# Optimization experiments

Hardware: AMD Instinct MI355X
Metric: run time of the kernel (lower is better)

The kernel has to match this reference:

```python
import jax, jax.numpy as jnp
import numpy as np

MASK_ID = 8192


def setup_inputs() -> dict:
    key = jax.random.key(0)
    k1, k2, k3, k4 = jax.random.split(key, 4)
    B, S, D = 8, 512, 1024
    x = jax.random.normal(k1, (B, S, D), dtype=jnp.float32) * 0.05
    embedding = jax.random.normal(k2, (B, S, D), dtype=jnp.float32) * 0.05
    tok = jax.random.randint(k3, (B, S), 0, MASK_ID)
    is_masked = jax.random.uniform(k4, (B, S)) < 0.15
    masked_target = jnp.where(is_masked, MASK_ID, tok).astype(jnp.int64)
    return {"x": x, "embedding": embedding, "masked_target": masked_target}


def reference(x, embedding, masked_target):
    # x, embedding: [B, S, D]; masked_target: [B, S]
    B, S, D = x.shape
    mask = (masked_target == MASK_ID)                      # [B, S]
    # numerator logit: f . m per position
    numer = jnp.sum(embedding * x, axis=-1)                # [B, S]
    # denominator: each query f against ALL B*S hidden states
    keys = x.reshape(B * S, D)                             # [N, D]
    scores = jnp.einsum('bsd,nd->bsn', embedding, keys)    # [B, S, N]
    lse = jax.nn.logsumexp(scores, axis=-1)                # [B, S]
    # log(exp(numer) / sum(exp(scores))) == numer - lse
    per_tok = numer - lse
    count = jnp.sum(mask).astype(x.dtype)
    loss = jnp.sum(jnp.where(mask, per_tok, jnp.zeros_like(per_tok)))
    return -(loss / count)
```

## Files before the change

kernel.cpp:

```cpp
#include <hip/hip_runtime.h>
#include <hip/hip_bf16.h>
#include <stdint.h>

constexpr int N_TOK  = 4096;
constexpr int D_DIM  = 1024;
constexpr int MASK_ID_V = 8192;

constexpr int BM2  = 256;
constexpr int KIT  = D_DIM / 128;
constexpr int NSL2 = N_TOK / BM2;
constexpr int NPART = NSL2 * 4;

constexpr float SCALE   = 64.0f;
constexpr float INVSC2  = 1.0f / (SCALE * SCALE);

constexpr int BM = 128, BN = 128, BK = 64;
constexpr int KST = D_DIM / BK;
constexpr int NSLICE_FB = 8;
constexpr int SLICE_W   = N_TOK / NSLICE_FB;
constexpr int CTS       = SLICE_W / BN;
constexpr int LDW       = BK + 8;
constexpr int NPART_FB  = NSLICE_FB * 2;

constexpr int FIN_BLOCKS = 256;

typedef __attribute__((ext_vector_type(4)))  float f32x4;
typedef __attribute__((ext_vector_type(16))) float f32x16;
typedef __attribute__((ext_vector_type(8)))  short bf16x8;
typedef __attribute__((ext_vector_type(8)))  int   i32x8;

__device__ __forceinline__ uint32_t pk2bf(float lo, float hi) {
    union { float f; uint32_t u; } a, b;
    a.f = lo; b.f = hi;
    uint32_t ua = (a.u + 0x7fffu + ((a.u >> 16) & 1u)) >> 16;
    uint32_t ub = (b.u + 0x7fffu + ((b.u >> 16) & 1u)) >> 16;
    return ua | (ub << 16);
}

__device__ __forceinline__ void async16(void* lds, const void* g) {
    __builtin_amdgcn_global_load_lds(
        (const __attribute__((address_space(1))) uint32_t*)g,
        (__attribute__((address_space(3))) uint32_t*)lds,
        16, 0, 0);
}

#define BAR do { __builtin_amdgcn_s_barrier(); __builtin_amdgcn_sched_barrier(0); } while (0)

__device__ __forceinline__ uint pk4fp8(float4 v) {
    int w = __builtin_amdgcn_cvt_pk_fp8_f32(v.x * SCALE, v.y * SCALE, 0, false);
    w = __builtin_amdgcn_cvt_pk_fp8_f32(v.z * SCALE, v.w * SCALE, w, true);
    return (uint)w;
}

__global__ __launch_bounds__(256) void conv_fp8(
    const float* __restrict__ x, const float* __restrict__ e,
    unsigned char* __restrict__ xb8, unsigned char* __restrict__ eb8)
{
    constexpr int NC = N_TOK * D_DIM / 16;
    const int t0 = blockIdx.x * blockDim.x + threadIdx.x;
    const int stride = gridDim.x * blockDim.x;
    for (int c = t0; c < NC; c += stride) {
        const float4* px = (const float4*)x + (size_t)c * 4;
        uint4 o;
        o.x = pk4fp8(px[0]); o.y = pk4fp8(px[1]);
        o.z = pk4fp8(px[2]); o.w = pk4fp8(px[3]);
        ((uint4*)xb8)[c] = o;

        const float4* pe = (const float4*)e + (size_t)c * 4;
        uint4 q;
        q.x = pk4fp8(pe[0]); q.y = pk4fp8(pe[1]);
        q.z = pk4fp8(pe[2]); q.w = pk4fp8(pe[3]);
        ((uint4*)eb8)[c] = q;
    }
}

__device__ __forceinline__ i32x8 ld_frag(const unsigned char* base, int o0, int o1) {
    uint4 u = *(const uint4*)(base + o0);
    uint4 v = *(const uint4*)(base + o1);
    i32x8 r = { (int)u.x, (int)u.y, (int)u.z, (int)u.w,
                (int)v.x, (int)v.y, (int)v.z, (int)v.w };
    return r;
}

#define MFMA8(A_, B_, C_) __builtin_amdgcn_mfma_scale_f32_32x32x64_f8f6f4( \
    A_, B_, C_, 0, 0, 0, 127, 0, 127)

__global__ __launch_bounds__(1024, 4) void nce_gemm_fp8(
    const unsigned char* __restrict__ xb8,
    const unsigned char* __restrict__ eb8,
    float* __restrict__ numer,
    float* __restrict__ ps)
{
    __shared__ unsigned char As[2][32768];
    __shared__ unsigned char Bs[2][32768];

    const int bid   = blockIdx.x;
    const int sw    = (bid & 7) * 32 + (bid >> 3);
    const int chunk = sw >> 4, win = sw & 15;
    const int rb    = (chunk & 3) * 4 + (win & 3);
    const int cs    = (chunk >> 2) * 4 + (win >> 2);
    const int row0  = rb * BM2;
    const int col0  = cs * BM2;

    const int tid  = threadIdx.x;
    const int lane = tid & 63;
    const int wid  = tid >> 6;
    const int wr   = wid >> 2;
    const int wc   = wid & 3;
    const int l31  = lane & 31;
    const int lg   = lane >> 5;

    const int q0_ = wid * 128 + lane;
    const int q1_ = q0_ + 64;
    const int r0_ = q0_ >> 3, c0_ = (q0_ & 7) ^ (r0_ & 7);
    const int r1_ = q1_ >> 3, c1_ = (q1_ & 7) ^ (r1_ & 7);
    const unsigned char* gA0 = eb8 + (size_t)(row0 + r0_) * D_DIM + c0_ * 16;
    const unsigned char* gA1 = eb8 + (size_t)(row0 + r1_) * D_DIM + c1_ * 16;
    const unsigned char* gB0 = xb8 + (size_t)(col0 + r0_) * D_DIM + c0_ * 16;
    const unsigned char* gB1 = xb8 + (size_t)(col0 + r1_) * D_DIM + c1_ * 16;

    const int rA = wr * 64 + l31;
    const int pA = (lg * 2) ^ (rA & 7);
    const int rB = wc * 64 + l31;
    const int pB = (lg * 2) ^ (rB & 7);
    int offA[2][2], offB[2][2];
#pragma unroll
    for (int ks = 0; ks < 2; ++ks)
#pragma unroll
        for (int j = 0; j < 2; ++j) {
            offA[ks][j] = rA * 128 + ((pA ^ (ks << 2) ^ j) << 4);
            offB[ks][j] = rB * 128 + ((pB ^ (ks << 2) ^ j) << 4);
        }

    f32x16 acc00, acc01, acc10, acc11;
#pragma unroll
    for (int i = 0; i < 16; ++i) { acc00[i] = 0.f; acc01[i] = 0.f; acc10[i] = 0.f; acc11[i] = 0.f; }

    async16(As[0] + wid * 2048,        gA0);
    async16(As[0] + wid * 2048 + 1024, gA1);
    async16(Bs[0] + wid * 2048,        gB0);
    async16(Bs[0] + wid * 2048 + 1024, gB1);

#pragma unroll 1
    for (int kt = 0; kt < KIT; ++kt) {
        const int c = kt & 1, n = c ^ 1;

        asm volatile("s_waitcnt vmcnt(0)" ::: "memory");
        BAR;

        if (kt < KIT - 1) {
            const int ko = (kt + 1) * 128;
            async16(As[n] + wid * 2048,        gA0 + ko);
            async16(As[n] + wid * 2048 + 1024, gA1 + ko);
            async16(Bs[n] + wid * 2048,        gB0 + ko);
            async16(Bs[n] + wid * 2048 + 1024, gB1 + ko);
        }

        const unsigned char* Ab = As[c];
        const unsigned char* Bb = Bs[c];
#pragma unroll
        for (int ks = 0; ks < 2; ++ks) {
            i32x8 a0 = ld_frag(Ab,        offA[ks][0], offA[ks][1]);
            i32x8 a1 = ld_frag(Ab + 4096, offA[ks][0], offA[ks][1]);
            i32x8 b0 = ld_frag(Bb,        offB[ks][0], offB[ks][1]);
            i32x8 b1 = ld_frag(Bb + 4096, offB[ks][0], offB[ks][1]);
            __builtin_amdgcn_s_setprio(1);
            acc00 = MFMA8(a0, b0, acc00);
            acc01 = MFMA8(a0, b1, acc01);
            acc10 = MFMA8(a1, b0, acc10);
            acc11 = MFMA8(a1, b1, acc11);
            __builtin_amdgcn_s_setprio(0);
        }
    }

    const int c0g = col0 + wc * 64 + l31;
    const int c1g = c0g + 32;

#pragma unroll
    for (int reg = 0; reg < 16; ++reg) {
        const int rif = (reg & 3) + 8 * (reg >> 2) + 4 * lg;
#pragma unroll
        for (int fr = 0; fr < 2; ++fr) {
            const int row_g = row0 + wr * 64 + fr * 32 + rif;
            const float v0 = (fr ? acc10[reg] : acc00[reg]) * INVSC2;
            const float v1 = (fr ? acc11[reg] : acc01[reg]) * INVSC2;
            if (row_g == c0g) numer[row_g] = v0;
            if (row_g == c1g) numer[row_g] = v1;
            float s = __expf(v0) + __expf(v1);
#pragma unroll
            for (int off = 1; off <= 16; off <<= 1)
                s += __shfl_xor(s, off, 64);
            if (l31 == 0)
                ps[row_g * NPART + cs * 4 + wc] = s;
        }
    }
}

__global__ __launch_bounds__(256) void nce_finish_a2(
    const int* __restrict__ tgt,
    const float* __restrict__ numer,
    const float* __restrict__ ps,
    float* __restrict__ bl_loss,
    float* __restrict__ bl_cnt)
{
    const int tid  = threadIdx.x;
    const int lane = tid & 63;
    const int wv   = tid >> 6;
    const int waves_total = gridDim.x * 4;

    float loss = 0.f, cnt = 0.f;

    for (int row = blockIdx.x * 4 + wv; row < N_TOK; row += waves_total) {
        if (tgt[row] != MASK_ID_V) continue;
        float sv = (lane < NPART) ? ps[row * NPART + lane] : 0.f;
#pragma unroll
        for (int off = 32; off; off >>= 1) sv += __shfl_xor(sv, off, 64);
        if (lane == 0) {
            loss += numer[row] - __logf(sv);
            cnt  += 1.f;
        }
    }

    __shared__ float sl[4], sc[4];
    if (lane == 0) { sl[wv] = loss; sc[wv] = cnt; }
    __syncthreads();
    if (tid == 0) {
        bl_loss[blockIdx.x] = sl[0] + sl[1] + sl[2] + sl[3];
        bl_cnt[blockIdx.x]  = sc[0] + sc[1] + sc[2] + sc[3];
    }
}

__global__ __launch_bounds__(256) void nce_finish_a(
    const int* __restrict__ tgt,
    const float* __restrict__ numer,
    const float* __restrict__ pm,
    const float* __restrict__ ps,
    float* __restrict__ bl_loss,
    float* __restrict__ bl_cnt,
    int npart)
{
    const int tid  = threadIdx.x;
    const int lane = tid & 63;
    const int wv   = tid >> 6;
    const int waves_total = gridDim.x * 4;

    float loss = 0.f, cnt = 0.f;

    for (int row = blockIdx.x * 4 + wv; row < N_TOK; row += waves_total) {
        if (tgt[row] != MASK_ID_V) continue;
        float pmv = -3.0e38f, psv = 0.f;
        if (lane < npart) {
            pmv = pm[row * npart + lane];
            psv = ps[row * npart + lane];
        }
        float m = pmv;
#pragma unroll
        for (int off = 32; off; off >>= 1) m = fmaxf(m, __shfl_xor(m, off, 64));
        float sv = psv * __expf(pmv - m);
#pragma unroll
        for (int off = 32; off; off >>= 1) sv += __shfl_xor(sv, off, 64);
        if (lane == 0) {
            loss += numer[row] - (m + __logf(sv));
            cnt  += 1.f;
        }
    }

    __shared__ float sl[4], sc[4];
    if (lane == 0) { sl[wv] = loss; sc[wv] = cnt; }
    __syncthreads();
    if (tid == 0) {
        bl_loss[blockIdx.x] = sl[0] + sl[1] + sl[2] + sl[3];
        bl_cnt[blockIdx.x]  = sc[0] + sc[1] + sc[2] + sc[3];
    }
}

__global__ __launch_bounds__(256) void nce_finish_b(
    const float* __restrict__ bl_loss,
    const float* __restrict__ bl_cnt,
    float* __restrict__ out, int nblk)
{
    const int tid = threadIdx.x;
    float l = 0.f, c = 0.f;
    for (int i = tid; i < nblk; i += 256) { l += bl_loss[i]; c += bl_cnt[i]; }
    __shared__ float sl[256], sc[256];
    sl[tid] = l; sc[tid] = c;
    __syncthreads();
    for (int off = 128; off; off >>= 1) {
        if (tid < off) { sl[tid] += sl[tid + off]; sc[tid] += sc[tid + off]; }
        __syncthreads();
    }
    if (tid == 0) out[0] = -(sl[0] / sc[0]);
}

__global__ __launch_bounds__(256, 2) void nce_gemm_fb(
    const float* __restrict__ x, const float* __restrict__ emb,
    float* __restrict__ numer, float* __restrict__ pm, float* __restrict__ ps)
{
    __shared__ ushort At[BM][LDW];
    __shared__ ushort Bt[BN][LDW];

    const int rb = blockIdx.x, cs = blockIdx.y;
    const int row0 = rb * BM, col0 = cs * SLICE_W;
    const int tid = threadIdx.x, lane = tid & 63, wid = tid >> 6;
    const int wr = wid >> 1, wc = wid & 1, l15 = lane & 15, lhi = lane >> 4;

    float m_run[16], s_run[16];
#pragma unroll
    for (int i = 0; i < 16; ++i) { m_run[i] = -3.0e38f; s_run[i] = 0.0f; }

    for (int ct = 0; ct < CTS; ++ct) {
        const int colt0 = col0 + ct * BN;
        f32x4 acc[4][4];
#pragma unroll
        for (int a = 0; a < 4; ++a)
#pragma unroll
            for (int b = 0; b < 4; ++b) acc[a][b] = f32x4{0.f,0.f,0.f,0.f};

#pragma unroll 1
        for (int kt = 0; kt < KST; ++kt) {
            __syncthreads();
#pragma unroll
            for (int i = 0; i < 4; ++i) {
                const int chunk = tid + i * 256;
                const int r = chunk >> 3, c8 = (chunk & 7) << 3;
                const float* ga = emb + (size_t)(row0 + r) * D_DIM + kt * BK + c8;
                float4 a0 = *(const float4*)(ga); float4 a1 = *(const float4*)(ga + 4);
                uint4 pa;
                pa.x = pk2bf(a0.x, a0.y); pa.y = pk2bf(a0.z, a0.w);
                pa.z = pk2bf(a1.x, a1.y); pa.w = pk2bf(a1.z, a1.w);
                *(uint4*)&At[r][c8] = pa;
                const float* gb = x + (size_t)(colt0 + r) * D_DIM + kt * BK + c8;
                float4 b0 = *(const float4*)(gb); float4 b1 = *(const float4*)(gb + 4);
                uint4 pb;
                pb.x = pk2bf(b0.x, b0.y); pb.y = pk2bf(b0.z, b0.w);
                pb.z = pk2bf(b1.x, b1.y); pb.w = pk2bf(b1.z, b1.w);
                *(uint4*)&Bt[r][c8] = pb;
            }
            __syncthreads();
#pragma unroll
            for (int kp = 0; kp < 2; ++kp) {
                const int ko = kp * 32 + lhi * 8;
                bf16x8 af[4], bfr[4];
#pragma unroll
                for (int mi = 0; mi < 4; ++mi)
                    af[mi] = *(const bf16x8*)&At[wr*64 + mi*16 + l15][ko];
#pragma unroll
                for (int ni = 0; ni < 4; ++ni)
                    bfr[ni] = *(const bf16x8*)&Bt[wc*64 + ni*16 + l15][ko];
#pragma unroll
                for (int mi = 0; mi < 4; ++mi)
#pragma unroll
                    for (int ni = 0; ni < 4; ++ni)
                        acc[mi][ni] = __builtin_amdgcn_mfma_f32_16x16x32_bf16(
                            af[mi], bfr[ni], acc[mi][ni], 0, 0, 0);
            }
        }

#pragma unroll
        for (int mi = 0; mi < 4; ++mi)
#pragma unroll
            for (int r = 0; r < 4; ++r) {
                const int row_g = row0 + wr*64 + mi*16 + lhi*4 + r;
#pragma unroll
                for (int ni = 0; ni < 4; ++ni) {
                    const int col_g = colt0 + wc*64 + ni*16 + l15;
                    if (row_g == col_g) numer[row_g] = acc[mi][ni][r];
                }
                const int idx = mi * 4 + r;
                const float v0 = acc[mi][0][r], v1 = acc[mi][1][r];
                const float v2 = acc[mi][2][r], v3 = acc[mi][3][r];
                const float mx = fmaxf(fmaxf(v0, v1), fmaxf(v2, v3));
                const float mn = fmaxf(m_run[idx], mx);
                const float scale = __expf(m_run[idx] - mn);
                s_run[idx] = s_run[idx] * scale
                           + __expf(v0 - mn) + __expf(v1 - mn)
                           + __expf(v2 - mn) + __expf(v3 - mn);
                m_run[idx] = mn;
            }
    }

#pragma unroll
    for (int idx = 0; idx < 16; ++idx) {
        float m = m_run[idx], s = s_run[idx];
#pragma unroll
        for (int off = 1; off < 16; off <<= 1) {
            const float mo = __shfl_xor(m, off, 64);
            const float so = __shfl_xor(s, off, 64);
            const float mn = fmaxf(m, mo);
            s = s * __expf(m - mn) + so * __expf(mo - mn);
            m = mn;
        }
        m_run[idx] = m; s_run[idx] = s;
    }

    if (l15 == 0) {
        const int slot = cs * 2 + wc;
#pragma unroll
        for (int mi = 0; mi < 4; ++mi)
#pragma unroll
            for (int r = 0; r < 4; ++r) {
                const int row_g = row0 + wr*64 + mi*16 + lhi*4 + r;
                pm[row_g * NPART_FB + slot] = m_run[mi*4 + r];
                ps[row_g * NPART_FB + slot] = s_run[mi*4 + r];
            }
    }
}

extern "C" void kernel_launch(void* const* d_in, const int* in_sizes, int n_in,
                              void* d_out, int out_size, void* d_ws, size_t ws_size,
                              hipStream_t stream) {
    (void)in_sizes; (void)n_in; (void)out_size;
    const float* x   = (const float*)d_in[0];
    const float* emb = (const float*)d_in[1];
    const int*   tgt = (const int*)d_in[2];
    float* out = (float*)d_out;

    const size_t elems = (size_t)N_TOK * D_DIM;
    const size_t need  = elems * 2
                       + (size_t)N_TOK * 4
                       + (size_t)N_TOK * NPART * 4
                       + FIN_BLOCKS * 8;

    if (ws_size >= need) {
        unsigned char* xb8 = (unsigned char*)d_ws;
        unsigned char* eb8 = xb8 + elems;
        float* numer = (float*)(eb8 + elems);
        float* ps    = numer + N_TOK;
        float* bl    = ps + (size_t)N_TOK * NPART;
        float* bc    = bl + FIN_BLOCKS;

        conv_fp8<<<1024, 256, 0, stream>>>(x, emb, xb8, eb8);
        nce_gemm_fp8<<<NSL2 * NSL2, 1024, 0, stream>>>(xb8, eb8, numer, ps);
        nce_finish_a2<<<FIN_BLOCKS, 256, 0, stream>>>(tgt, numer, ps, bl, bc);
        nce_finish_b<<<1, 256, 0, stream>>>(bl, bc, out, FIN_BLOCKS);
    } else {
        float* numer = (float*)d_ws;
        float* pm    = numer + N_TOK;
        float* ps    = pm + (size_t)N_TOK * NPART_FB;
        float* bl    = ps + (size_t)N_TOK * NPART_FB;
        float* bc    = bl + FIN_BLOCKS;
        nce_gemm_fb<<<dim3(N_TOK / BM, NSLICE_FB), 256, 0, stream>>>(x, emb, numer, pm, ps);
        nce_finish_a<<<FIN_BLOCKS, 256, 0, stream>>>(tgt, numer, pm, ps, bl, bc, NPART_FB);
        nce_finish_b<<<1, 256, 0, stream>>>(bl, bc, out, FIN_BLOCKS);
    }
}
```

Baseline: 41.94 us.

## Quantize operands to FP4 with MFMA-fragment-ordered layout for the NCE GEMM

Replaces the FP8 conversion and GEMM with an FP4 (e2m1) path. A custom encoder writes the data pre-arranged in MFMA fragment order, so the GEMM loads fragments with one contiguous 16-byte read and no swizzle. This halves operand bytes and LDS footprint and uses the FP4 mode of the scaled MFMA. In exchange, FP4 with a fixed scale of 25 greatly reduces dot-product precision, which risks the loss accuracy, and the branch-heavy encoder adds conversion ALU work.

```diff
diff --git a/kernel.cpp b/kernel.cpp
--- a/kernel.cpp
+++ b/kernel.cpp
@@ -11,8 +11,8 @@
 constexpr int NSL2 = N_TOK / BM2;
 constexpr int NPART = NSL2 * 4;
 
-constexpr float SCALE   = 64.0f;
-constexpr float INVSC2  = 1.0f / (SCALE * SCALE);
+constexpr float SCALE4  = 25.0f;
+constexpr float INVSC4  = 1.0f / (SCALE4 * SCALE4);
 
 constexpr int BM = 128, BN = 128, BK = 64;
 constexpr int KST = D_DIM / BK;
@@ -46,53 +46,72 @@
 
 #define BAR do { __builtin_amdgcn_s_barrier(); __builtin_amdgcn_sched_barrier(0); } while (0)
 
-__device__ __forceinline__ uint pk4fp8(float4 v) {
-    int w = __builtin_amdgcn_cvt_pk_fp8_f32(v.x * SCALE, v.y * SCALE, 0, false);
-    w = __builtin_amdgcn_cvt_pk_fp8_f32(v.z * SCALE, v.w * SCALE, w, true);
-    return (uint)w;
-}
-
-__global__ __launch_bounds__(256) void conv_fp8(
+__device__ __forceinline__ uint enc8fp4(const float* s) {
+    uint w = 0;
+#pragma unroll
+    for (int i = 0; i < 8; ++i) {
+        const float v = s[i] * SCALE4;
+        const uint sgn = (__float_as_uint(v) >> 31) << 3;
+        const float a = fminf(fabsf(v), 6.0f);
+        const uint c = (a >= 0.25f) + (a >= 0.75f) + (a >= 1.25f)
+                     + (a >= 1.75f) + (a >= 2.5f)  + (a >= 3.5f)
+                     + (a >= 5.0f);
+        w |= (sgn | c) << (4 * i);
+    }
+    return w;
+}
+
+__global__ __launch_bounds__(256) void conv_fp4(
     const float* __restrict__ x, const float* __restrict__ e,
-    unsigned char* __restrict__ xb8, unsigned char* __restrict__ eb8)
-{
-    constexpr int NC = N_TOK * D_DIM / 16;
+    unsigned char* __restrict__ xb4, unsigned char* __restrict__ eb4)
+{
+    constexpr int NCH   = (N_TOK / 32) * 16;
+    constexpr int NTASK = NCH * 64;
     const int t0 = blockIdx.x * blockDim.x + threadIdx.x;
     const int stride = gridDim.x * blockDim.x;
-    for (int c = t0; c < NC; c += stride) {
-        const float4* px = (const float4*)x + (size_t)c * 4;
-        uint4 o;
-        o.x = pk4fp8(px[0]); o.y = pk4fp8(px[1]);
-        o.z = pk4fp8(px[2]); o.w = pk4fp8(px[3]);
-        ((uint4*)xb8)[c] = o;
-
-        const float4* pe = (const float4*)e + (size_t)c * 4;
-        uint4 q;
-        q.x = pk4fp8(pe[0]); q.y = pk4fp8(pe[1]);
-        q.z = pk4fp8(pe[2]); q.w = pk4fp8(pe[3]);
-        ((uint4*)eb8)[c] = q;
-    }
-}
-
-__device__ __forceinline__ i32x8 ld_frag(const unsigned char* base, int o0, int o1) {
-    uint4 u = *(const uint4*)(base + o0);
-    uint4 v = *(const uint4*)(base + o1);
-    i32x8 r = { (int)u.x, (int)u.y, (int)u.z, (int)u.w,
-                (int)v.x, (int)v.y, (int)v.z, (int)v.w };
+    for (int t = t0; t < NTASK; t += stride) {
+        const int c  = t >> 6, l = t & 63;
+        const int R  = c >> 4;
+        const int kt = (c >> 1) & 7;
+        const int ks = c & 1;
+        const int row = R * 32 + (l & 31);
+        const int col = kt * 128 + ks * 64 + (l >> 5) * 32;
+        const size_t src = (size_t)row * D_DIM + col;
+        const size_t dst = (size_t)c * 1024 + (size_t)l * 16;
+
+        float bx[32], be[32];
+#pragma unroll
+        for (int j = 0; j < 8; ++j) {
+            ((float4*)bx)[j] = *(const float4*)(x + src + j * 4);
+            ((float4*)be)[j] = *(const float4*)(e + src + j * 4);
+        }
+        uint4 ox, oe;
+        ox.x = enc8fp4(bx);      ox.y = enc8fp4(bx + 8);
+        ox.z = enc8fp4(bx + 16); ox.w = enc8fp4(bx + 24);
+        oe.x = enc8fp4(be);      oe.y = enc8fp4(be + 8);
+        oe.z = enc8fp4(be + 16); oe.w = enc8fp4(be + 24);
+        *(uint4*)(xb4 + dst) = ox;
+        *(uint4*)(eb4 + dst) = oe;
+    }
+}
+
+__device__ __forceinline__ i32x8 ld_fp4(const unsigned char* p) {
+    uint4 u = *(const uint4*)(p);
+    i32x8 r = { (int)u.x, (int)u.y, (int)u.z, (int)u.w, 0, 0, 0, 0 };
     return r;
 }
 
-#define MFMA8(A_, B_, C_) __builtin_amdgcn_mfma_scale_f32_32x32x64_f8f6f4( \
-    A_, B_, C_, 0, 0, 0, 127, 0, 127)
-
-__global__ __launch_bounds__(1024, 4) void nce_gemm_fp8(
-    const unsigned char* __restrict__ xb8,
-    const unsigned char* __restrict__ eb8,
+#define MFMA4(A_, B_, C_) __builtin_amdgcn_mfma_scale_f32_32x32x64_f8f6f4( \
+    A_, B_, C_, 4, 4, 0, 127, 0, 127)
+
+__global__ __launch_bounds__(1024, 4) void nce_gemm_fp4(
+    const unsigned char* __restrict__ xb4,
+    const unsigned char* __restrict__ eb4,
     float* __restrict__ numer,
     float* __restrict__ ps)
 {
-    __shared__ unsigned char As[2][32768];
-    __shared__ unsigned char Bs[2][32768];
+    __shared__ unsigned char As[2][16384];
+    __shared__ unsigned char Bs[2][16384];
 
     const int bid   = blockIdx.x;
     const int sw    = (bid & 7) * 32 + (bid >> 3);
@@ -110,36 +129,21 @@
     const int l31  = lane & 31;
     const int lg   = lane >> 5;
 
-    const int q0_ = wid * 128 + lane;
-    const int q1_ = q0_ + 64;
-    const int r0_ = q0_ >> 3, c0_ = (q0_ & 7) ^ (r0_ & 7);
-    const int r1_ = q1_ >> 3, c1_ = (q1_ & 7) ^ (r1_ & 7);
-    const unsigned char* gA0 = eb8 + (size_t)(row0 + r0_) * D_DIM + c0_ * 16;
-    const unsigned char* gA1 = eb8 + (size_t)(row0 + r1_) * D_DIM + c1_ * 16;
-    const unsigned char* gB0 = xb8 + (size_t)(col0 + r0_) * D_DIM + c0_ * 16;
-    const unsigned char* gB1 = xb8 + (size_t)(col0 + r1_) * D_DIM + c1_ * 16;
-
-    const int rA = wr * 64 + l31;
-    const int pA = (lg * 2) ^ (rA & 7);
-    const int rB = wc * 64 + l31;
-    const int pB = (lg * 2) ^ (rB & 7);
-    int offA[2][2], offB[2][2];
-#pragma unroll
-    for (int ks = 0; ks < 2; ++ks)
-#pragma unroll
-        for (int j = 0; j < 2; ++j) {
-            offA[ks][j] = rA * 128 + ((pA ^ (ks << 2) ^ j) << 4);
-            offB[ks][j] = rB * 128 + ((pB ^ (ks << 2) ^ j) << 4);
-        }
+    const unsigned char* sA = eb4 +
+        ((size_t)(rb * 8 + (wid >> 1)) * 16 + (wid & 1)) * 1024 + (size_t)lane * 16;
+    const unsigned char* sB = xb4 +
+        ((size_t)(cs * 8 + (wid >> 1)) * 16 + (wid & 1)) * 1024 + (size_t)lane * 16;
+    const int dLds = wid * 1024;
+
+    const int aBase = wr * 4096 + lane * 16;
+    const int bBase = wc * 4096 + lane * 16;
 
     f32x16 acc00, acc01, acc10, acc11;
 #pragma unroll
     for (int i = 0; i < 16; ++i) { acc00[i] = 0.f; acc01[i] = 0.f; acc10[i] = 0.f; acc11[i] = 0.f; }
 
-    async16(As[0] + wid * 2048,        gA0);
-    async16(As[0] + wid * 2048 + 1024, gA1);
-    async16(Bs[0] + wid * 2048,        gB0);
-    async16(Bs[0] + wid * 2048 + 1024, gB1);
+    async16(As[0] + dLds, sA);
+    async16(Bs[0] + dLds, sB);
 
 #pragma unroll 1
     for (int kt = 0; kt < KIT; ++kt) {
@@ -149,26 +153,24 @@
         BAR;
 
         if (kt < KIT - 1) {
-            const int ko = (kt + 1) * 128;
-            async16(As[n] + wid * 2048,        gA0 + ko);
-            async16(As[n] + wid * 2048 + 1024, gA1 + ko);
-            async16(Bs[n] + wid * 2048,        gB0 + ko);
-            async16(Bs[n] + wid * 2048 + 1024, gB1 + ko);
-        }
-
-        const unsigned char* Ab = As[c];
-        const unsigned char* Bb = Bs[c];
+            const size_t ko = (size_t)(kt + 1) * 2048;
+            async16(As[n] + dLds, sA + ko);
+            async16(Bs[n] + dLds, sB + ko);
+        }
+
+        const unsigned char* Ab = As[c] + aBase;
+        const unsigned char* Bb = Bs[c] + bBase;
 #pragma unroll
         for (int ks = 0; ks < 2; ++ks) {
-            i32x8 a0 = ld_frag(Ab,        offA[ks][0], offA[ks][1]);
-            i32x8 a1 = ld_frag(Ab + 4096, offA[ks][0], offA[ks][1]);
-            i32x8 b0 = ld_frag(Bb,        offB[ks][0], offB[ks][1]);
-            i32x8 b1 = ld_frag(Bb + 4096, offB[ks][0], offB[ks][1]);
+            i32x8 a0 = ld_fp4(Ab + ks * 1024);
+            i32x8 a1 = ld_fp4(Ab + 2048 + ks * 1024);
+            i32x8 b0 = ld_fp4(Bb + ks * 1024);
+            i32x8 b1 = ld_fp4(Bb + 2048 + ks * 1024);
             __builtin_amdgcn_s_setprio(1);
-            acc00 = MFMA8(a0, b0, acc00);
-            acc01 = MFMA8(a0, b1, acc01);
-            acc10 = MFMA8(a1, b0, acc10);
-            acc11 = MFMA8(a1, b1, acc11);
+            acc00 = MFMA4(a0, b0, acc00);
+            acc01 = MFMA4(a0, b1, acc01);
+            acc10 = MFMA4(a1, b0, acc10);
+            acc11 = MFMA4(a1, b1, acc11);
             __builtin_amdgcn_s_setprio(0);
         }
     }
@@ -182,8 +184,8 @@
 #pragma unroll
         for (int fr = 0; fr < 2; ++fr) {
             const int row_g = row0 + wr * 64 + fr * 32 + rif;
-            const float v0 = (fr ? acc10[reg] : acc00[reg]) * INVSC2;
-            const float v1 = (fr ? acc11[reg] : acc01[reg]) * INVSC2;
+            const float v0 = (fr ? acc10[reg] : acc00[reg]) * INVSC4;
+            const float v1 = (fr ? acc11[reg] : acc01[reg]) * INVSC4;
             if (row_g == c0g) numer[row_g] = v0;
             if (row_g == c1g) numer[row_g] = v1;
             float s = __expf(v0) + __expf(v1);
@@ -416,21 +418,21 @@
     float* out = (float*)d_out;
 
     const size_t elems = (size_t)N_TOK * D_DIM;
-    const size_t need  = elems * 2
+    const size_t need  = elems
                        + (size_t)N_TOK * 4
                        + (size_t)N_TOK * NPART * 4
                        + FIN_BLOCKS * 8;
 
     if (ws_size >= need) {
-        unsigned char* xb8 = (unsigned char*)d_ws;
-        unsigned char* eb8 = xb8 + elems;
-        float* numer = (float*)(eb8 + elems);
+        unsigned char* xb4 = (unsigned char*)d_ws;
+        unsigned char* eb4 = xb4 + elems / 2;
+        float* numer = (float*)(eb4 + elems / 2);
         float* ps    = numer + N_TOK;
         float* bl    = ps + (size_t)N_TOK * NPART;
         float* bc    = bl + FIN_BLOCKS;
 
-        conv_fp8<<<1024, 256, 0, stream>>>(x, emb, xb8, eb8);
-        nce_gemm_fp8<<<NSL2 * NSL2, 1024, 0, stream>>>(xb8, eb8, numer, ps);
+        conv_fp4<<<512, 256, 0, stream>>>(x, emb, xb4, eb4);
+        nce_gemm_fp4<<<NSL2 * NSL2, 1024, 0, stream>>>(xb4, eb4, numer, ps);
         nce_finish_a2<<<FIN_BLOCKS, 256, 0, stream>>>(tgt, numer, ps, bl, bc);
         nce_finish_b<<<1, 256, 0, stream>>>(bl, bc, out, FIN_BLOCKS);
     } else {
```

After: 37.26 us. 1.13x faster.
